# Optimization experiments

Measured on AMD Instinct MI355X. Metric: run time of the kernel, lower is better.

Reference implementation:

```python
import jax, jax.numpy as jnp
from jax import lax
import numpy as np

B, T, I, H = 64, 2048, 256, 256


def setup_inputs() -> dict:
    key = jax.random.key(0)
    k_x, k_h, k_wi, k_bi, k_wh, k_bh = jax.random.split(key, 6)
    si = 1.0 / np.sqrt(I)
    sh = 1.0 / np.sqrt(H)
    return {
        "x": jax.random.normal(k_x, (B, T, I), dtype=jnp.float32),
        "h0": jax.random.normal(k_h, (B, H), dtype=jnp.float32),
        "W_ih": jax.random.uniform(k_wi, (3 * H, I), dtype=jnp.float32, minval=-si, maxval=si),
        "b_ih": jax.random.uniform(k_bi, (3 * H,), dtype=jnp.float32, minval=-si, maxval=si),
        "W_hh": jax.random.uniform(k_wh, (3 * H, H), dtype=jnp.float32, minval=-sh, maxval=sh),
        "b_hh": jax.random.uniform(k_bh, (3 * H,), dtype=jnp.float32, minval=-sh, maxval=sh),
    }


def reference(x, h0, W_ih, b_ih, W_hh, b_hh):
    # batch_first=True -> transpose to time-major [T, B, I]
    xt = jnp.transpose(x, (1, 0, 2))
    # Batch the input-to-hidden projection across all timesteps (one big GEMM)
    gi = jnp.einsum("tbi,gi->tbg", xt, W_ih) + b_ih  # [T, B, 3H]

    def step(h, gi_t):
        gh = h @ W_hh.T + b_hh                     # [B, 3H]
        i_r, i_c, i_u = jnp.split(gi_t, 3, axis=1)
        h_r, h_c, h_u = jnp.split(gh, 3, axis=1)
        u = jax.nn.sigmoid(i_u + h_u)              # update gate
        r = jax.nn.sigmoid(i_r + h_r)              # reset gate
        n = jnp.tanh(i_c + r * h_c)                # candidate state
        hy = (1.0 - u) * h + u * n
        return hy, hy

    hN, out = lax.scan(step, h0, gi)               # out: [T, B, H]
    return jnp.transpose(out, (1, 0, 2)), hN       # ([B, T, H], [B, H])
```

## Files before the change

kernel.cpp:

```cpp
#include <hip/hip_runtime.h>
#include <cstdint>
#include <cstddef>

#define B_ 64
#define T_ 2048
#define I_ 256
#define H_ 256
#define G_ 768

typedef _Float16 h2v __attribute__((ext_vector_type(2)));
typedef _Float16 v8h __attribute__((ext_vector_type(8)));
typedef float    v4f __attribute__((ext_vector_type(4)));
typedef uint32_t u32x4 __attribute__((ext_vector_type(4)));

union U32h { uint32_t u; h2v h; };

__global__ void prep_whh_frag(const float* __restrict__ Whh, uint32_t* __restrict__ Wp) {
    int rt = blockIdx.x;
    int kb = blockIdx.y;
    int lane = threadIdx.x;
    int r16 = lane & 15, hi2 = lane >> 4;
    const float* src = Whh + (size_t)(rt * 16 + r16) * 256 + kb * 32 + hi2 * 8;
    uint32_t d[4];
    for (int p = 0; p < 4; ++p) {
        U32h u; u.h = h2v{(_Float16)src[2 * p], (_Float16)src[2 * p + 1]};
        d[p] = u.u;
    }
    *(u32x4*)(Wp + (((size_t)rt * 8 + kb) * 64 + lane) * 4) = u32x4{d[0], d[1], d[2], d[3]};
}

#define LDA 56
#define LDB 56

__launch_bounds__(256, 2)
__global__ void gemm_gi(const float* __restrict__ x, const float* __restrict__ Wih,
                        const float* __restrict__ bih, _Float16* __restrict__ gi,
                        int t0) {
    __shared__ __align__(16) _Float16 As[64 * LDA];
    __shared__ __align__(16) _Float16 Bs[384 * LDB];
    int tid  = threadIdx.x;
    int t    = t0 + blockIdx.x;
    int n0   = blockIdx.y * 384;
    int lane = tid & 63, wave = tid >> 6;
    int quad = lane >> 4, r16 = lane & 15;

    v4f acc[24];
#pragma unroll
    for (int i = 0; i < 24; ++i) acc[i] = v4f{0.f, 0.f, 0.f, 0.f};

    for (int ki = 0; ki < 8; ++ki) {
        int k0 = ki * 32;
        __syncthreads();
#pragma unroll
        for (int s = 0; s < 2; ++s) {
            int slot = tid + s * 256;
            int row = slot >> 3;
            int part = slot & 7;
            const float* xp = x + ((size_t)row * T_ + t) * I_ + k0 + part * 4;
            float4 v = *(const float4*)xp;
            U32h u0, u1;
            u0.h = h2v{(_Float16)v.x, (_Float16)v.y};
            u1.h = h2v{(_Float16)v.z, (_Float16)v.w};
            uint32_t* dst = (uint32_t*)&As[row * LDA + part * 4];
            dst[0] = u0.u; dst[1] = u1.u;
        }
#pragma unroll
        for (int s = 0; s < 12; ++s) {
            int slot = tid + s * 256;
            int row = slot >> 3;
            int part = slot & 7;
            const float* wp = Wih + (size_t)(n0 + row) * I_ + k0 + part * 4;
            float4 v = *(const float4*)wp;
            U32h u0, u1;
            u0.h = h2v{(_Float16)v.x, (_Float16)v.y};
            u1.h = h2v{(_Float16)v.z, (_Float16)v.w};
            uint32_t* dst = (uint32_t*)&Bs[row * LDB + part * 4];
            dst[0] = u0.u; dst[1] = u1.u;
        }
        __syncthreads();
        v8h af = *(const v8h*)&As[(wave * 16 + r16) * LDA + quad * 8];
#pragma unroll
        for (int nt = 0; nt < 24; ++nt) {
            v8h bf = *(const v8h*)&Bs[(nt * 16 + r16) * LDB + quad * 8];
            acc[nt] = __builtin_amdgcn_mfma_f32_16x16x32_f16(af, bf, acc[nt], 0, 0, 0);
        }
    }
#pragma unroll
    for (int nt = 0; nt < 24; ++nt) {
        int n = n0 + nt * 16 + r16;
        float bias = bih[n];
#pragma unroll
        for (int reg = 0; reg < 4; ++reg) {
            int m = wave * 16 + quad * 4 + reg;
            size_t off = ((size_t)blockIdx.x * 64 + m) * G_ + n;
            gi[off] = (_Float16)(acc[nt][reg] + bias);
        }
    }
}

__global__ void __launch_bounds__(512, 1)
rec_step(const v8h* __restrict__ Wfrag, const float* __restrict__ bhh,
         const _Float16* __restrict__ gi, const float* __restrict__ h_init,
         float* __restrict__ out, float* __restrict__ hN,
         float* __restrict__ h_carry, int t0, int len) {
    __shared__ __align__(16) _Float16 hb[2][256];
    __shared__ __align__(16) float ypart[G_];

    int b = blockIdx.x;
    int tid = threadIdx.x;
    int lane = tid & 63, wave = tid >> 6;
    int r16 = lane & 15, hi2 = lane >> 4;
    int j = tid & 255;

    v8h w[48];
#pragma unroll
    for (int f = 0; f < 48; ++f) {
        int rt = wave * 6 + (f >> 3);
        int kb = f & 7;
        w[f] = Wfrag[((size_t)rt * 8 + kb) * 64 + lane];
    }

    float bh0 = 0.f, bh1 = 0.f, bh2 = 0.f, hprev = 0.f;
    float g0 = 0.f, g1 = 0.f, g2 = 0.f;
    const _Float16* gp = gi + (size_t)b * G_ + j;
    float* outp = out + (size_t)b * T_ * H_ + (size_t)t0 * H_ + j;
    if (tid < 256) {
        bh0 = bhh[j]; bh1 = bhh[256 + j]; bh2 = bhh[512 + j];
        hprev = h_init[b * 256 + j];
        hb[0][j] = (_Float16)hprev;
        g0 = (float)gp[0]; g1 = (float)gp[256]; g2 = (float)gp[512];
    }
    __syncthreads();

    int cur = 0;
    for (int t = 0; t < len; ++t) {
        float p0 = 0.f, p1 = 0.f, p2 = 0.f;
        if (tid < 256 && t + 1 < len) {
            const _Float16* gq = gp + (size_t)(t + 1) * B_ * G_;
            p0 = (float)gq[0]; p1 = (float)gq[256]; p2 = (float)gq[512];
        }

        v8h bf[8];
#pragma unroll
        for (int kb = 0; kb < 8; ++kb)
            bf[kb] = *(const v8h*)&hb[cur][kb * 32 + hi2 * 8];

#pragma unroll
        for (int r = 0; r < 6; ++r) {
            v4f acc = v4f{0.f, 0.f, 0.f, 0.f};
#pragma unroll
            for (int kb = 0; kb < 8; ++kb)
                acc = __builtin_amdgcn_mfma_f32_16x16x32_f16(w[r * 8 + kb], bf[kb], acc, 0, 0, 0);
            if (r16 == 0)
                *(v4f*)&ypart[(wave * 6 + r) * 16 + hi2 * 4] = acc;
        }
        __syncthreads();

        if (tid < 256) {
            float s0 = ypart[j]       + bh0;
            float s1 = ypart[256 + j] + bh1;
            float s2 = ypart[512 + j] + bh2;
            float r = 1.f / (1.f + __expf(-(g0 + s0)));
            float u = 1.f / (1.f + __expf(-(g2 + s2)));
            float carg = g1 + r * s1;
            carg = fminf(fmaxf(carg, -20.f), 20.f);
            float e2 = __expf(2.f * carg);
            float n = (e2 - 1.f) / (e2 + 1.f);
            float hnew = hprev + u * (n - hprev);
            outp[(size_t)t * H_] = hnew;
            hb[cur ^ 1][j] = (_Float16)hnew;
            hprev = hnew;
            g0 = p0; g1 = p1; g2 = p2;
        }
        __syncthreads();
        cur ^= 1;
    }
    if (tid < 256) {
        h_carry[b * 256 + j] = hprev;
        if (t0 + len == T_) hN[b * 256 + j] = hprev;
    }
}

extern "C" void kernel_launch(void* const* d_in, const int* in_sizes, int n_in,
                              void* d_out, int out_size, void* d_ws, size_t ws_size,
                              hipStream_t stream) {
    const float* x   = (const float*)d_in[0];
    const float* h0  = (const float*)d_in[1];
    const float* Wih = (const float*)d_in[2];
    const float* bih = (const float*)d_in[3];
    const float* Whh = (const float*)d_in[4];
    const float* bhh = (const float*)d_in[5];
    float* out = (float*)d_out;
    float* hN  = out + (size_t)B_ * T_ * H_;

    char* ws = (char*)d_ws;
    float*    h_carry = (float*)ws;
    uint32_t* Wprep   = (uint32_t*)(ws + 65536);
    _Float16* gi      = (_Float16*)(ws + 65536 + 393216);

    const size_t head = 65536 + 393216;
    const size_t per_t = (size_t)B_ * G_ * sizeof(_Float16);
    size_t avail = (ws_size > head) ? (ws_size - head) : 0;
    int tc = (int)(avail / per_t);
    if (tc > T_) tc = T_;
    if (tc < 1)  tc = 1;
    int nch = (T_ + tc - 1) / tc;
    tc = (T_ + nch - 1) / nch;

    hipLaunchKernelGGL(prep_whh_frag, dim3(48, 8), dim3(64), 0, stream, Whh, Wprep);
    for (int t0 = 0; t0 < T_; t0 += tc) {
        int len = (T_ - t0 < tc) ? (T_ - t0) : tc;
        hipLaunchKernelGGL(gemm_gi, dim3(len, 2), dim3(256), 0, stream,
                           x, Wih, bih, gi, t0);
        const float* hi = (t0 == 0) ? h0 : h_carry;
        hipLaunchKernelGGL(rec_step, dim3(64), dim3(512), 0, stream,
                           (const v8h*)Wprep, bhh, gi, hi, out, hN, h_carry, t0, len);
    }
}
```

Before: 3.144 ms.

## Hand-write GRU recurrence loop in inline assembly with fused biases

Replaces the compiled recurrent step loop with a hand-scheduled inline-assembly loop. It keeps the W_hh fragments pinned in VGPRs, interleaves three independent MFMA accumulator chains with LDS reads of h, and computes the gates with raw exp/rcp and a tanh built from a sigmoid. The r and u recurrent biases are folded into the input-projection GEMM, and all 512 threads run the gate math, with the high half writing harmlessly to a dump buffer. The goal is less per-step latency on the serial critical path. In exchange, correctness now depends on fixed register usage, manual nops and wait counts, and the loop assumes len is at least 1.

Result: slower. 3.370 ms (+7.2%).

```diff
diff --git a/kernel.cpp b/kernel.cpp
--- a/kernel.cpp
+++ b/kernel.cpp
@@ -34,8 +34,8 @@
 
 __launch_bounds__(256, 2)
 __global__ void gemm_gi(const float* __restrict__ x, const float* __restrict__ Wih,
-                        const float* __restrict__ bih, _Float16* __restrict__ gi,
-                        int t0) {
+                        const float* __restrict__ bih, const float* __restrict__ bhh,
+                        _Float16* __restrict__ gi, int t0) {
     __shared__ __align__(16) _Float16 As[64 * LDA];
     __shared__ __align__(16) _Float16 Bs[384 * LDB];
     int tid  = threadIdx.x;
@@ -88,7 +88,7 @@
 #pragma unroll
     for (int nt = 0; nt < 24; ++nt) {
         int n = n0 + nt * 16 + r16;
-        float bias = bih[n];
+        float bias = bih[n] + ((n < 256 || n >= 512) ? bhh[n] : 0.0f);
 #pragma unroll
         for (int reg = 0; reg < 4; ++reg) {
             int m = wave * 16 + quad * 4 + reg;
@@ -98,13 +98,14 @@
     }
 }
 
-__global__ void __launch_bounds__(512, 1)
-rec_step(const v8h* __restrict__ Wfrag, const float* __restrict__ bhh,
+__global__ void __launch_bounds__(512)
+rec_step(const uint32_t* __restrict__ Wfrag, const float* __restrict__ bhh,
          const _Float16* __restrict__ gi, const float* __restrict__ h_init,
          float* __restrict__ out, float* __restrict__ hN,
          float* __restrict__ h_carry, int t0, int len) {
-    __shared__ __align__(16) _Float16 hb[2][256];
+    __shared__ __align__(1024) _Float16 hb[2][256];
     __shared__ __align__(16) float ypart[G_];
+    __shared__ __align__(16) float dump[2176];
 
     int b = blockIdx.x;
     int tid = threadIdx.x;
@@ -112,72 +113,311 @@
     int r16 = lane & 15, hi2 = lane >> 4;
     int j = tid & 255;
 
-    v8h w[48];
-#pragma unroll
-    for (int f = 0; f < 48; ++f) {
-        int rt = wave * 6 + (f >> 3);
-        int kb = f & 7;
-        w[f] = Wfrag[((size_t)rt * 8 + kb) * 64 + lane];
-    }
-
-    float bh0 = 0.f, bh1 = 0.f, bh2 = 0.f, hprev = 0.f;
-    float g0 = 0.f, g1 = 0.f, g2 = 0.f;
-    const _Float16* gp = gi + (size_t)b * G_ + j;
-    float* outp = out + (size_t)b * T_ * H_ + (size_t)t0 * H_ + j;
+    uint32_t ldsHb = (uint32_t)(uintptr_t)&hb[0][0];
+    uint32_t ldsYp = (uint32_t)(uintptr_t)&ypart[0];
+    uint32_t ldsDp = (uint32_t)(uintptr_t)&dump[0];
+
+    uint32_t hrd = ldsHb + hi2 * 16;
+    uint32_t hwr = ldsHb + 512 + j * 2;
+    uint32_t ypw = (r16 == 0) ? (ldsYp + wave * 384 + hi2 * 16)
+                              : (ldsDp + (wave * 64 + lane) * 16);
+    uint32_t ypr = ldsYp + j * 4;
+
+    uint64_t wad = (uint64_t)(uintptr_t)Wfrag + ((uint64_t)wave * 48 * 64 + lane) * 16;
+    uint64_t oad = (uint64_t)(uintptr_t)out + (((uint64_t)b * T_ + t0) * H_ + j) * 4;
+    uint64_t gad = (uint64_t)(uintptr_t)gi + ((uint64_t)b * G_ + j) * 2;
+
+    float hp  = h_init[b * 256 + j];
+    float bh1 = bhh[256 + j];
+    if (tid < 256) hb[0][j] = (_Float16)hp;
+    __syncthreads();
+
+    float hout;
+    asm volatile(
+        "v_lshlrev_b64 v[40:41], 0, %[oad]\n\t"
+        "v_lshlrev_b64 v[42:43], 0, %[gad]\n\t"
+        "v_lshlrev_b64 v[28:29], 0, %[wad]\n\t"
+        "v_mov_b32 v36, %[hrd]\n\t"
+        "v_mov_b32 v37, %[ypw]\n\t"
+        "v_mov_b32 v38, %[ypr]\n\t"
+        "v_mov_b32 v39, %[hwr]\n\t"
+        "v_mov_b32 v51, %[bh1]\n\t"
+        "v_mov_b32 v47, %[hp]\n\t"
+        "s_mov_b32 s80, %[len]\n\t"
+        "global_load_dwordx4 v[64:67], v[28:29], off\n\t"
+        "global_load_dwordx4 v[68:71], v[28:29], off offset:1024\n\t"
+        "global_load_dwordx4 v[72:75], v[28:29], off offset:2048\n\t"
+        "global_load_dwordx4 v[76:79], v[28:29], off offset:3072\n\t"
+        "v_add_co_u32 v28, vcc, 0x1000, v28\n\t"
+        "v_addc_co_u32 v29, vcc, 0, v29, vcc\n\t"
+        "global_load_dwordx4 v[80:83], v[28:29], off\n\t"
+        "global_load_dwordx4 v[84:87], v[28:29], off offset:1024\n\t"
+        "global_load_dwordx4 v[88:91], v[28:29], off offset:2048\n\t"
+        "global_load_dwordx4 v[92:95], v[28:29], off offset:3072\n\t"
+        "v_add_co_u32 v28, vcc, 0x1000, v28\n\t"
+        "v_addc_co_u32 v29, vcc, 0, v29, vcc\n\t"
+        "global_load_dwordx4 v[96:99], v[28:29], off\n\t"
+        "global_load_dwordx4 v[100:103], v[28:29], off offset:1024\n\t"
+        "global_load_dwordx4 v[104:107], v[28:29], off offset:2048\n\t"
+        "global_load_dwordx4 v[108:111], v[28:29], off offset:3072\n\t"
+        "v_add_co_u32 v28, vcc, 0x1000, v28\n\t"
+        "v_addc_co_u32 v29, vcc, 0, v29, vcc\n\t"
+        "global_load_dwordx4 v[112:115], v[28:29], off\n\t"
+        "global_load_dwordx4 v[116:119], v[28:29], off offset:1024\n\t"
+        "global_load_dwordx4 v[120:123], v[28:29], off offset:2048\n\t"
+        "global_load_dwordx4 v[124:127], v[28:29], off offset:3072\n\t"
+        "v_add_co_u32 v28, vcc, 0x1000, v28\n\t"
+        "v_addc_co_u32 v29, vcc, 0, v29, vcc\n\t"
+        "global_load_dwordx4 v[128:131], v[28:29], off\n\t"
+        "global_load_dwordx4 v[132:135], v[28:29], off offset:1024\n\t"
+        "global_load_dwordx4 v[136:139], v[28:29], off offset:2048\n\t"
+        "global_load_dwordx4 v[140:143], v[28:29], off offset:3072\n\t"
+        "v_add_co_u32 v28, vcc, 0x1000, v28\n\t"
+        "v_addc_co_u32 v29, vcc, 0, v29, vcc\n\t"
+        "global_load_dwordx4 v[144:147], v[28:29], off\n\t"
+        "global_load_dwordx4 v[148:151], v[28:29], off offset:1024\n\t"
+        "global_load_dwordx4 v[152:155], v[28:29], off offset:2048\n\t"
+        "global_load_dwordx4 v[156:159], v[28:29], off offset:3072\n\t"
+        "v_add_co_u32 v28, vcc, 0x1000, v28\n\t"
+        "v_addc_co_u32 v29, vcc, 0, v29, vcc\n\t"
+        "global_load_dwordx4 v[160:163], v[28:29], off\n\t"
+        "global_load_dwordx4 v[164:167], v[28:29], off offset:1024\n\t"
+        "global_load_dwordx4 v[168:171], v[28:29], off offset:2048\n\t"
+        "global_load_dwordx4 v[172:175], v[28:29], off offset:3072\n\t"
+        "v_add_co_u32 v28, vcc, 0x1000, v28\n\t"
+        "v_addc_co_u32 v29, vcc, 0, v29, vcc\n\t"
+        "global_load_dwordx4 v[176:179], v[28:29], off\n\t"
+        "global_load_dwordx4 v[180:183], v[28:29], off offset:1024\n\t"
+        "global_load_dwordx4 v[184:187], v[28:29], off offset:2048\n\t"
+        "global_load_dwordx4 v[188:191], v[28:29], off offset:3072\n\t"
+        "v_add_co_u32 v28, vcc, 0x1000, v28\n\t"
+        "v_addc_co_u32 v29, vcc, 0, v29, vcc\n\t"
+        "global_load_dwordx4 v[192:195], v[28:29], off\n\t"
+        "global_load_dwordx4 v[196:199], v[28:29], off offset:1024\n\t"
+        "global_load_dwordx4 v[200:203], v[28:29], off offset:2048\n\t"
+        "global_load_dwordx4 v[204:207], v[28:29], off offset:3072\n\t"
+        "v_add_co_u32 v28, vcc, 0x1000, v28\n\t"
+        "v_addc_co_u32 v29, vcc, 0, v29, vcc\n\t"
+        "global_load_dwordx4 v[208:211], v[28:29], off\n\t"
+        "global_load_dwordx4 v[212:215], v[28:29], off offset:1024\n\t"
+        "global_load_dwordx4 v[216:219], v[28:29], off offset:2048\n\t"
+        "global_load_dwordx4 v[220:223], v[28:29], off offset:3072\n\t"
+        "v_add_co_u32 v28, vcc, 0x1000, v28\n\t"
+        "v_addc_co_u32 v29, vcc, 0, v29, vcc\n\t"
+        "global_load_dwordx4 v[224:227], v[28:29], off\n\t"
+        "global_load_dwordx4 v[228:231], v[28:29], off offset:1024\n\t"
+        "global_load_dwordx4 v[232:235], v[28:29], off offset:2048\n\t"
+        "global_load_dwordx4 v[236:239], v[28:29], off offset:3072\n\t"
+        "v_add_co_u32 v28, vcc, 0x1000, v28\n\t"
+        "v_addc_co_u32 v29, vcc, 0, v29, vcc\n\t"
+        "global_load_dwordx4 v[240:243], v[28:29], off\n\t"
+        "global_load_dwordx4 v[244:247], v[28:29], off offset:1024\n\t"
+        "global_load_dwordx4 v[248:251], v[28:29], off offset:2048\n\t"
+        "global_load_dwordx4 v[252:255], v[28:29], off offset:3072\n\t"
+        "global_load_ushort v48, v[42:43], off\n\t"
+        "global_load_ushort v49, v[42:43], off offset:512\n\t"
+        "global_load_ushort v50, v[42:43], off offset:1024\n\t"
+        "v_add_co_u32 v42, vcc, 0x18000, v42\n\t"
+        "v_addc_co_u32 v43, vcc, 0, v43, vcc\n\t"
+        "s_waitcnt vmcnt(0)\n\t"
+        "v_cvt_f32_f16 v44, v48\n\t"
+        "v_cvt_f32_f16 v45, v49\n\t"
+        "v_cvt_f32_f16 v46, v50\n\t"
+        "s_nop 3\n\t"
+        "9:\n\t"
+        "global_load_ushort v48, v[42:43], off\n\t"
+        "global_load_ushort v49, v[42:43], off offset:512\n\t"
+        "global_load_ushort v50, v[42:43], off offset:1024\n\t"
+        "v_mov_b32 v52, 0\n\t" "v_mov_b32 v53, 0\n\t" "v_mov_b32 v54, 0\n\t" "v_mov_b32 v55, 0\n\t"
+        "v_mov_b32 v56, 0\n\t" "v_mov_b32 v57, 0\n\t" "v_mov_b32 v58, 0\n\t" "v_mov_b32 v59, 0\n\t"
+        "v_mov_b32 v60, 0\n\t" "v_mov_b32 v61, 0\n\t" "v_mov_b32 v62, 0\n\t" "v_mov_b32 v63, 0\n\t"
+        "ds_read_b128 v[28:31], v36\n\t"
+        "ds_read_b128 v[32:35], v36 offset:64\n\t"
+        "s_waitcnt lgkmcnt(1)\n\t"
+        "v_mfma_f32_16x16x32_f16 v[52:55], v[64:67], v[28:31], v[52:55]\n\t"
+        "v_mfma_f32_16x16x32_f16 v[56:59], v[96:99], v[28:31], v[56:59]\n\t"
+        "v_mfma_f32_16x16x32_f16 v[60:63], v[128:131], v[28:31], v[60:63]\n\t"
+        "ds_read_b128 v[28:31], v36 offset:128\n\t"
+        "s_waitcnt lgkmcnt(1)\n\t"
+        "v_mfma_f32_16x16x32_f16 v[52:55], v[68:71], v[32:35], v[52:55]\n\t"
+        "v_mfma_f32_16x16x32_f16 v[56:59], v[100:103], v[32:35], v[56:59]\n\t"
+        "v_mfma_f32_16x16x32_f16 v[60:63], v[132:135], v[32:35], v[60:63]\n\t"
+        "ds_read_b128 v[32:35], v36 offset:192\n\t"
+        "s_waitcnt lgkmcnt(1)\n\t"
+        "v_mfma_f32_16x16x32_f16 v[52:55], v[72:75], v[28:31], v[52:55]\n\t"
+        "v_mfma_f32_16x16x32_f16 v[56:59], v[104:107], v[28:31], v[56:59]\n\t"
+        "v_mfma_f32_16x16x32_f16 v[60:63], v[136:139], v[28:31], v[60:63]\n\t"
+        "ds_read_b128 v[28:31], v36 offset:256\n\t"
+        "s_waitcnt lgkmcnt(1)\n\t"
+        "v_mfma_f32_16x16x32_f16 v[52:55], v[76:79], v[32:35], v[52:55]\n\t"
+        "v_mfma_f32_16x16x32_f16 v[56:59], v[108:111], v[32:35], v[56:59]\n\t"
+        "v_mfma_f32_16x16x32_f16 v[60:63], v[140:143], v[32:35], v[60:63]\n\t"
+        "ds_read_b128 v[32:35], v36 offset:320\n\t"
+        "s_waitcnt lgkmcnt(1)\n\t"
+        "v_mfma_f32_16x16x32_f16 v[52:55], v[80:83], v[28:31], v[52:55]\n\t"
+        "v_mfma_f32_16x16x32_f16 v[56:59], v[112:115], v[28:31], v[56:59]\n\t"
+        "v_mfma_f32_16x16x32_f16 v[60:63], v[144:147], v[28:31], v[60:63]\n\t"
+        "ds_read_b128 v[28:31], v36 offset:384\n\t"
+        "s_waitcnt lgkmcnt(1)\n\t"
+        "v_mfma_f32_16x16x32_f16 v[52:55], v[84:87], v[32:35], v[52:55]\n\t"
+        "v_mfma_f32_16x16x32_f16 v[56:59], v[116:119], v[32:35], v[56:59]\n\t"
+        "v_mfma_f32_16x16x32_f16 v[60:63], v[148:151], v[32:35], v[60:63]\n\t"
+        "ds_read_b128 v[32:35], v36 offset:448\n\t"
+        "s_waitcnt lgkmcnt(1)\n\t"
+        "v_mfma_f32_16x16x32_f16 v[52:55], v[88:91], v[28:31], v[52:55]\n\t"
+        "v_mfma_f32_16x16x32_f16 v[56:59], v[120:123], v[28:31], v[56:59]\n\t"
+        "v_mfma_f32_16x16x32_f16 v[60:63], v[152:155], v[28:31], v[60:63]\n\t"
+        "s_waitcnt lgkmcnt(0)\n\t"
+        "v_mfma_f32_16x16x32_f16 v[52:55], v[92:95], v[32:35], v[52:55]\n\t"
+        "v_mfma_f32_16x16x32_f16 v[56:59], v[124:127], v[32:35], v[56:59]\n\t"
+        "v_mfma_f32_16x16x32_f16 v[60:63], v[156:159], v[32:35], v[60:63]\n\t"
+        "s_nop 7\n\t"
+        "s_nop 7\n\t"
+        "ds_write_b128 v37, v[52:55]\n\t"
+        "ds_write_b128 v37, v[56:59] offset:64\n\t"
+        "ds_write_b128 v37, v[60:63] offset:128\n\t"
+        "s_waitcnt lgkmcnt(0)\n\t"
+        "v_mov_b32 v52, 0\n\t" "v_mov_b32 v53, 0\n\t" "v_mov_b32 v54, 0\n\t" "v_mov_b32 v55, 0\n\t"
+        "v_mov_b32 v56, 0\n\t" "v_mov_b32 v57, 0\n\t" "v_mov_b32 v58, 0\n\t" "v_mov_b32 v59, 0\n\t"
+        "v_mov_b32 v60, 0\n\t" "v_mov_b32 v61, 0\n\t" "v_mov_b32 v62, 0\n\t" "v_mov_b32 v63, 0\n\t"
+        "ds_read_b128 v[28:31], v36\n\t"
+        "ds_read_b128 v[32:35], v36 offset:64\n\t"
+        "s_waitcnt lgkmcnt(1)\n\t"
+        "v_mfma_f32_16x16x32_f16 v[52:55], v[160:163], v[28:31], v[52:55]\n\t"
+        "v_mfma_f32_16x16x32_f16 v[56:59], v[192:195], v[28:31], v[56:59]\n\t"
+        "v_mfma_f32_16x16x32_f16 v[60:63], v[224:227], v[28:31], v[60:63]\n\t"
+        "ds_read_b128 v[28:31], v36 offset:128\n\t"
+        "s_waitcnt lgkmcnt(1)\n\t"
+        "v_mfma_f32_16x16x32_f16 v[52:55], v[164:167], v[32:35], v[52:55]\n\t"
+        "v_mfma_f32_16x16x32_f16 v[56:59], v[196:199], v[32:35], v[56:59]\n\t"
+        "v_mfma_f32_16x16x32_f16 v[60:63], v[228:231], v[32:35], v[60:63]\n\t"
+        "ds_read_b128 v[32:35], v36 offset:192\n\t"
+        "s_waitcnt lgkmcnt(1)\n\t"
+        "v_mfma_f32_16x16x32_f16 v[52:55], v[168:171], v[28:31], v[52:55]\n\t"
+        "v_mfma_f32_16x16x32_f16 v[56:59], v[200:203], v[28:31], v[56:59]\n\t"
+        "v_mfma_f32_16x16x32_f16 v[60:63], v[232:235], v[28:31], v[60:63]\n\t"
+        "ds_read_b128 v[28:31], v36 offset:256\n\t"
+        "s_waitcnt lgkmcnt(1)\n\t"
+        "v_mfma_f32_16x16x32_f16 v[52:55], v[172:175], v[32:35], v[52:55]\n\t"
+        "v_mfma_f32_16x16x32_f16 v[56:59], v[204:207], v[32:35], v[56:59]\n\t"
+        "v_mfma_f32_16x16x32_f16 v[60:63], v[236:239], v[32:35], v[60:63]\n\t"
+        "ds_read_b128 v[32:35], v36 offset:320\n\t"
+        "s_waitcnt lgkmcnt(1)\n\t"
+        "v_mfma_f32_16x16x32_f16 v[52:55], v[176:179], v[28:31], v[52:55]\n\t"
+        "v_mfma_f32_16x16x32_f16 v[56:59], v[208:211], v[28:31], v[56:59]\n\t"
+        "v_mfma_f32_16x16x32_f16 v[60:63], v[240:243], v[28:31], v[60:63]\n\t"
+        "ds_read_b128 v[28:31], v36 offset:384\n\t"
+        "s_waitcnt lgkmcnt(1)\n\t"
+        "v_mfma_f32_16x16x32_f16 v[52:55], v[180:183], v[32:35], v[52:55]\n\t"
+        "v_mfma_f32_16x16x32_f16 v[56:59], v[212:215], v[32:35], v[56:59]\n\t"
+        "v_mfma_f32_16x16x32_f16 v[60:63], v[244:247], v[32:35], v[60:63]\n\t"
+        "ds_read_b128 v[32:35], v36 offset:448\n\t"
+        "s_waitcnt lgkmcnt(1)\n\t"
+        "v_mfma_f32_16x16x32_f16 v[52:55], v[184:187], v[28:31], v[52:55]\n\t"
+        "v_mfma_f32_16x16x32_f16 v[56:59], v[216:219], v[28:31], v[56:59]\n\t"
+        "v_mfma_f32_16x16x32_f16 v[60:63], v[248:251], v[28:31], v[60:63]\n\t"
+        "s_waitcnt lgkmcnt(0)\n\t"
+        "v_mfma_f32_16x16x32_f16 v[52:55], v[188:191], v[32:35], v[52:55]\n\t"
+        "v_mfma_f32_16x16x32_f16 v[56:59], v[220:223], v[32:35], v[56:59]\n\t"
+        "v_mfma_f32_16x16x32_f16 v[60:63], v[252:255], v[32:35], v[60:63]\n\t"
+        "s_nop 7\n\t"
+        "s_nop 7\n\t"
+        "ds_write_b128 v37, v[52:55] offset:192\n\t"
+        "ds_write_b128 v37, v[56:59] offset:256\n\t"
+        "ds_write_b128 v37, v[60:63] offset:320\n\t"
+        "s_waitcnt lgkmcnt(0)\n\t"
+        "s_barrier\n\t"
+        "ds_read_b32 v28, v38\n\t"
+        "ds_read_b32 v29, v38 offset:1024\n\t"
+        "ds_read_b32 v30, v38 offset:2048\n\t"
+        "s_waitcnt lgkmcnt(0)\n\t"
+        "v_add_f32 v31, v44, v28\n\t"
+        "v_mul_f32 v31, 0xbfb8aa3b, v31\n\t"
+        "v_exp_f32 v31, v31\n\t"
+        "s_nop 1\n\t"
+        "v_add_f32 v31, 1.0, v31\n\t"
+        "v_rcp_f32 v31, v31\n\t"
+        "s_nop 1\n\t"
+        "v_add_f32 v32, v46, v30\n\t"
+        "v_mul_f32 v32, 0xbfb8aa3b, v32\n\t"
+        "v_exp_f32 v32, v32\n\t"
+        "s_nop 1\n\t"
+        "v_add_f32 v32, 1.0, v32\n\t"
+        "v_rcp_f32 v32, v32\n\t"
+        "s_nop 1\n\t"
+        "v_add_f32 v33, v29, v51\n\t"
+        "v_mov_b32 v34, v45\n\t"
+        "v_fmac_f32 v34, v31, v33\n\t"
+        "v_mul_f32 v34, 0x4038aa3b, v34\n\t"
+        "v_exp_f32 v34, v34\n\t"
+        "s_nop 1\n\t"
+        "v_add_f32 v34, 1.0, v34\n\t"
+        "v_rcp_f32 v34, v34\n\t"
+        "s_nop 1\n\t"
+        "v_mov_b32 v35, 1.0\n\t"
+        "v_fmac_f32 v35, -2.0, v34\n\t"
+        "v_sub_f32 v28, v35, v47\n\t"
+        "v_mov_b32 v29, v47\n\t"
+        "v_fmac_f32 v29, v32, v28\n\t"
+        "s_waitcnt vmcnt(0)\n\t"
+        "v_cvt_f32_f16 v44, v48\n\t"
+        "v_cvt_f32_f16 v45, v49\n\t"
+        "v_cvt_f32_f16 v46, v50\n\t"
+        "global_store_dword v[40:41], v29, off\n\t"
+        "v_add_co_u32 v40, vcc, 0x400, v40\n\t"
+        "v_addc_co_u32 v41, vcc, 0, v41, vcc\n\t"
+        "v_cvt_f16_f32 v30, v29\n\t"
+        "ds_write_b16 v39, v30\n\t"
+        "v_mov_b32 v47, v29\n\t"
+        "v_add_co_u32 v42, vcc, 0x18000, v42\n\t"
+        "v_addc_co_u32 v43, vcc, 0, v43, vcc\n\t"
+        "v_xor_b32 v36, 0x200, v36\n\t"
+        "v_xor_b32 v39, 0x200, v39\n\t"
+        "s_waitcnt lgkmcnt(0)\n\t"
+        "s_barrier\n\t"
+        "s_sub_u32 s80, s80, 1\n\t"
+        "s_cmp_lg_u32 s80, 0\n\t"
+        "s_cbranch_scc1 9b\n\t"
+        "s_waitcnt vmcnt(0) lgkmcnt(0)\n\t"
+        "v_mov_b32 %[hout], v47\n\t"
+        : [hout] "=v"(hout)
+        : [wad] "v"(wad), [oad] "v"(oad), [gad] "v"(gad),
+          [hrd] "v"(hrd), [ypw] "v"(ypw), [ypr] "v"(ypr), [hwr] "v"(hwr),
+          [bh1] "v"(bh1), [hp] "v"(hp), [len] "s"(len)
+        : "memory", "vcc", "scc", "s80",
+          "v28","v29","v30","v31","v32","v33","v34","v35",
+          "v36","v37","v38","v39","v40","v41","v42","v43",
+          "v44","v45","v46","v47","v48","v49","v50","v51",
+          "v52","v53","v54","v55","v56","v57","v58","v59",
+          "v60","v61","v62","v63","v64","v65","v66","v67",
+          "v68","v69","v70","v71","v72","v73","v74","v75",
+          "v76","v77","v78","v79","v80","v81","v82","v83",
+          "v84","v85","v86","v87","v88","v89","v90","v91",
+          "v92","v93","v94","v95","v96","v97","v98","v99",
+          "v100","v101","v102","v103","v104","v105","v106","v107",
+          "v108","v109","v110","v111","v112","v113","v114","v115",
+          "v116","v117","v118","v119","v120","v121","v122","v123",
+          "v124","v125","v126","v127","v128","v129","v130","v131",
+          "v132","v133","v134","v135","v136","v137","v138","v139",
+          "v140","v141","v142","v143","v144","v145","v146","v147",
+          "v148","v149","v150","v151","v152","v153","v154","v155",
+          "v156","v157","v158","v159","v160","v161","v162","v163",
+          "v164","v165","v166","v167","v168","v169","v170","v171",
+          "v172","v173","v174","v175","v176","v177","v178","v179",
+          "v180","v181","v182","v183","v184","v185","v186","v187",
+          "v188","v189","v190","v191","v192","v193","v194","v195",
+          "v196","v197","v198","v199","v200","v201","v202","v203",
+          "v204","v205","v206","v207","v208","v209","v210","v211",
+          "v212","v213","v214","v215","v216","v217","v218","v219",
+          "v220","v221","v222","v223","v224","v225","v226","v227",
+          "v228","v229","v230","v231","v232","v233","v234","v235",
+          "v236","v237","v238","v239","v240","v241","v242","v243",
+          "v244","v245","v246","v247","v248","v249","v250","v251",
+          "v252","v253","v254","v255");
+
     if (tid < 256) {
-        bh0 = bhh[j]; bh1 = bhh[256 + j]; bh2 = bhh[512 + j];
-        hprev = h_init[b * 256 + j];
-        hb[0][j] = (_Float16)hprev;
-        g0 = (float)gp[0]; g1 = (float)gp[256]; g2 = (float)gp[512];
-    }
-    __syncthreads();
-
-    int cur = 0;
-    for (int t = 0; t < len; ++t) {
-        float p0 = 0.f, p1 = 0.f, p2 = 0.f;
-        if (tid < 256 && t + 1 < len) {
-            const _Float16* gq = gp + (size_t)(t + 1) * B_ * G_;
-            p0 = (float)gq[0]; p1 = (float)gq[256]; p2 = (float)gq[512];
-        }
-
-        v8h bf[8];
-#pragma unroll
-        for (int kb = 0; kb < 8; ++kb)
-            bf[kb] = *(const v8h*)&hb[cur][kb * 32 + hi2 * 8];
-
-#pragma unroll
-        for (int r = 0; r < 6; ++r) {
-            v4f acc = v4f{0.f, 0.f, 0.f, 0.f};
-#pragma unroll
-            for (int kb = 0; kb < 8; ++kb)
-                acc = __builtin_amdgcn_mfma_f32_16x16x32_f16(w[r * 8 + kb], bf[kb], acc, 0, 0, 0);
-            if (r16 == 0)
-                *(v4f*)&ypart[(wave * 6 + r) * 16 + hi2 * 4] = acc;
-        }
-        __syncthreads();
-
-        if (tid < 256) {
-            float s0 = ypart[j]       + bh0;
-            float s1 = ypart[256 + j] + bh1;
-            float s2 = ypart[512 + j] + bh2;
-            float r = 1.f / (1.f + __expf(-(g0 + s0)));
-            float u = 1.f / (1.f + __expf(-(g2 + s2)));
-            float carg = g1 + r * s1;
-            carg = fminf(fmaxf(carg, -20.f), 20.f);
-            float e2 = __expf(2.f * carg);
-            float n = (e2 - 1.f) / (e2 + 1.f);
-            float hnew = hprev + u * (n - hprev);
-            outp[(size_t)t * H_] = hnew;
-            hb[cur ^ 1][j] = (_Float16)hnew;
-            hprev = hnew;
-            g0 = p0; g1 = p1; g2 = p2;
-        }
-        __syncthreads();
-        cur ^= 1;
-    }
-    if (tid < 256) {
-        h_carry[b * 256 + j] = hprev;
-        if (t0 + len == T_) hN[b * 256 + j] = hprev;
+        h_carry[b * 256 + j] = hout;
+        if (t0 + len == T_) hN[b * 256 + j] = hout;
     }
 }
 
@@ -201,6 +441,7 @@
     const size_t head = 65536 + 393216;
     const size_t per_t = (size_t)B_ * G_ * sizeof(_Float16);
     size_t avail = (ws_size > head) ? (ws_size - head) : 0;
+    if (avail > per_t) avail -= per_t;
     int tc = (int)(avail / per_t);
     if (tc > T_) tc = T_;
     if (tc < 1)  tc = 1;
@@ -211,9 +452,9 @@
     for (int t0 = 0; t0 < T_; t0 += tc) {
         int len = (T_ - t0 < tc) ? (T_ - t0) : tc;
         hipLaunchKernelGGL(gemm_gi, dim3(len, 2), dim3(256), 0, stream,
-                           x, Wih, bih, gi, t0);
+                           x, Wih, bih, bhh, gi, t0);
         const float* hi = (t0 == 0) ? h0 : h_carry;
         hipLaunchKernelGGL(rec_step, dim3(64), dim3(512), 0, stream,
-                           (const v8h*)Wprep, bhh, gi, hi, out, hN, h_carry, t0, len);
+                           Wprep, bhh, gi, hi, out, hN, h_carry, t0, len);
     }
 }
```
